# Kernel tuning notes

Measured on AMD Instinct MI355X. Metric: run time of the kernel, lower is better.

The kernel has to match this reference:

```python
import jax, jax.numpy as jnp
import numpy as np

BATCH = 256
INPUT_DIM = 64
LEVELS = 100
HV_DIM = 10000


def setup_inputs() -> dict:
    key = jax.random.key(0)
    kx, kb = jax.random.split(key)
    x = jax.random.uniform(kx, (BATCH, INPUT_DIM), dtype=jnp.float32)
    base = jax.random.normal(kb, (INPUT_DIM, LEVELS, HV_DIM), dtype=jnp.float32)
    # buffer is L2-normalized along hv_dim at construction time
    base = base / jnp.linalg.norm(base, axis=-1, keepdims=True)
    return {"x": x, "base_hvs": base}


def reference(x, base_hvs):
    D, L, H = base_hvs.shape
    B = x.shape[0]
    xn = jnp.clip(x * (L - 1), 0.0, float(L - 1))          # [B, D]
    lo = jnp.floor(xn).astype(jnp.int32)                    # [B, D]
    hi = jnp.clip(lo + 1, 0, L - 1)                         # [B, D]
    alpha = xn - lo.astype(x.dtype)                         # [B, D]

    def step(acc, inputs):
        bhv, l, h, a = inputs    # bhv: [L, H], l/h/a: [B]
        hv_low = bhv[l]          # [B, H] gather
        hv_high = bhv[h]         # [B, H] gather
        a = a[:, None]
        return acc + (1.0 - a) * hv_low + a * hv_high, None

    init = jnp.zeros((B, H), dtype=x.dtype)
    encoded, _ = jax.lax.scan(step, init, (base_hvs, lo.T, hi.T, alpha.T))
    return encoded / jnp.linalg.norm(encoded, axis=-1, keepdims=True)
```

## Files before the change

kernel.cpp:

```cpp
#include <hip/hip_runtime.h>
#include <hip/hip_bf16.h>

#define BATCH   256
#define DIMS    64
#define LEVELS  100
#define HVD     10000
#define WH      128
#define NHT     79
#define DSPLIT  8
#define DPER    8
#define TPB     512

typedef unsigned int  uint;
typedef unsigned short ushort;

#define PRM_OFF_BYTES (DSPLIT * BATCH * HVD * 2)

static __device__ __forceinline__ ushort f2bf(float f) {
    __hip_bfloat16 h = __float2bfloat16(f);
    return *reinterpret_cast<ushort*>(&h);
}

__global__ __launch_bounds__(256) void setup_kernel(
    const float* __restrict__ x, uint2* __restrict__ prm)
{
    const int i = blockIdx.x * 256 + threadIdx.x;
    if (i >= DIMS * BATCH) return;
    const int d = i >> 8;
    const int b = i & 255;
    float xv = x[b * DIMS + d];
    float xn = fminf(fmaxf(xv * (float)(LEVELS - 1), 0.0f), (float)(LEVELS - 1));
    float fl = floorf(xn);
    int   lo = (int)fl;
    int   hi = lo < LEVELS - 1 ? lo + 1 : LEVELS - 1;
    prm[i] = make_uint2((uint)(lo * WH * 4) | ((uint)(hi * WH * 4) << 16),
                        __float_as_uint(xn - fl));
}

__global__ __launch_bounds__(TPB, 4) void encode_kernel(
    const float* __restrict__ base,
    const uint2* __restrict__ prm,
    ushort*      __restrict__ partial)
{
    __shared__ float s_chunk[LEVELS * WH];

    const int tid   = threadIdx.x;
    const int w     = tid >> 6;
    const int lane  = tid & 63;
    const int htile = blockIdx.x;
    const int split = blockIdx.y;
    const int h0    = htile * WH;
    const int d0    = split * DPER;
    const int wvalid = (HVD - h0) < WH ? (HVD - h0) : WH;

    const int wu    = __builtin_amdgcn_readfirstlane(w);
    const int bbase = wu * 32;

    const int s   = lane >> 5;
    const int c   = lane & 31;
    const int cb  = c * 16;
    const int c4  = c * 4;
    const int srow = lane >> 5;
    const int scol = (lane & 31) * 4;

    float4 acc[16];
    #pragma unroll
    for (int j = 0; j < 16; ++j) acc[j] = make_float4(0.f, 0.f, 0.f, 0.f);

    #pragma unroll 1
    for (int dc = 0; dc < DPER; ++dc) {
        __syncthreads();

        const float* src = base + ((size_t)(d0 + dc) * LEVELS) * (size_t)HVD + h0;
        for (int p = w; p < LEVELS / 2; p += 8) {
            const float* g = src + (size_t)(2 * p + srow) * HVD + scol;
            if (scol < wvalid) {
                __builtin_amdgcn_global_load_lds(
                    (const __attribute__((address_space(1))) uint*)g,
                    (__attribute__((address_space(3))) uint*)&s_chunk[p * 2 * WH],
                    16, 0, 0);
            }
        }
        __syncthreads();

        const uint2* pr = prm + (size_t)(d0 + dc) * BATCH + bbase;

        #pragma unroll
        for (int jj = 0; jj < 16; ++jj) {
            const uint4 pq = *(const uint4*)(pr + 2 * jj);
            const uint  lohi = s ? pq.z : pq.x;
            const float a    = __uint_as_float(s ? pq.w : pq.y);
            const int   olo  = (int)(lohi & 0xffffu);
            const int   ohi  = (int)(lohi >> 16);
            const float4 vlo = *(const float4*)((const char*)s_chunk + olo + cb);
            const float4 vhi = *(const float4*)((const char*)s_chunk + ohi + cb);
            const float wl = 1.0f - a;
            acc[jj].x += wl * vlo.x + a * vhi.x;
            acc[jj].y += wl * vlo.y + a * vhi.y;
            acc[jj].z += wl * vlo.z + a * vhi.z;
            acc[jj].w += wl * vlo.w + a * vhi.w;
        }
    }

    if (c4 < wvalid) {
        #pragma unroll
        for (int jj = 0; jj < 16; ++jj) {
            const int b = bbase + 2 * jj + s;
            uint2 pk;
            pk.x = (uint)f2bf(acc[jj].x) | ((uint)f2bf(acc[jj].y) << 16);
            pk.y = (uint)f2bf(acc[jj].z) | ((uint)f2bf(acc[jj].w) << 16);
            *(uint2*)(partial + ((size_t)split * BATCH + b) * (size_t)HVD + h0 + c4) = pk;
        }
    }
}

__global__ __launch_bounds__(256) void finish_kernel(
    const ushort* __restrict__ partial,
    float* __restrict__ out)
{
    const int b   = blockIdx.x;
    const int tid = threadIdx.x;

    float ss = 0.f;
    for (int i = tid; i < HVD / 4; i += 256) {
        float4 sum = make_float4(0.f, 0.f, 0.f, 0.f);
        #pragma unroll
        for (int sp = 0; sp < DSPLIT; ++sp) {
            const uint2 u = *(const uint2*)(partial +
                ((size_t)sp * BATCH + b) * (size_t)HVD + i * 4);
            sum.x += __uint_as_float(u.x << 16);
            sum.y += __uint_as_float(u.x & 0xffff0000u);
            sum.z += __uint_as_float(u.y << 16);
            sum.w += __uint_as_float(u.y & 0xffff0000u);
        }
        *(float4*)(out + (size_t)b * HVD + i * 4) = sum;
        ss += sum.x * sum.x + sum.y * sum.y + sum.z * sum.z + sum.w * sum.w;
    }

    __shared__ float red[256];
    red[tid] = ss;
    __syncthreads();
    #pragma unroll
    for (int sh = 128; sh > 0; sh >>= 1) {
        if (tid < sh) red[tid] += red[tid + sh];
        __syncthreads();
    }
    const float inv = rsqrtf(red[0]);

    for (int i = tid; i < HVD / 4; i += 256) {
        float4 v = *(float4*)(out + (size_t)b * HVD + i * 4);
        v.x *= inv; v.y *= inv; v.z *= inv; v.w *= inv;
        *(float4*)(out + (size_t)b * HVD + i * 4) = v;
    }
}

extern "C" void kernel_launch(void* const* d_in, const int* in_sizes, int n_in,
                              void* d_out, int out_size, void* d_ws, size_t ws_size,
                              hipStream_t stream)
{
    const float* x    = (const float*)d_in[0];
    const float* base = (const float*)d_in[1];
    float*       out  = (float*)d_out;
    ushort*      part = (ushort*)d_ws;
    uint2*       prm  = (uint2*)((char*)d_ws + PRM_OFF_BYTES);

    setup_kernel<<<DIMS, 256, 0, stream>>>(x, prm);
    dim3 grid(NHT, DSPLIT);
    encode_kernel<<<grid, TPB, 0, stream>>>(base, prm, part);
    finish_kernel<<<BATCH, 256, 0, stream>>>(part, out);
}
```

Measured before the change: 383.4 us.

## Double-buffer LDS level chunks with async loads and narrower hv tiles

The encode kernel now uses 64-wide hv tiles and 256 threads per block. It keeps two LDS buffers so the global-to-LDS load for dimension dc+2 is in flight while dc is being accumulated, using vmcnt waits and raw barriers in place of full syncthreads. Per-sample parameters are packed into one 32-bit word (fp16 alpha plus 8-bit lo and hi indices) and staged once into LDS per block. This aims to hide global load latency behind compute, at the cost of reduced alpha precision, doubled LDS use per block, and narrower float2 LDS reads.

```diff
diff --git a/kernel.cpp b/kernel.cpp
--- a/kernel.cpp
+++ b/kernel.cpp
@@ -1,17 +1,20 @@
 #include <hip/hip_runtime.h>
+#include <hip/hip_fp16.h>
 #include <hip/hip_bf16.h>
 
 #define BATCH   256
 #define DIMS    64
 #define LEVELS  100
 #define HVD     10000
-#define WH      128
-#define NHT     79
+#define WH      64
+#define NHT     157
 #define DSPLIT  8
 #define DPER    8
-#define TPB     512
+#define TPB     256
+#define CHUNK_FLOATS (LEVELS * WH)
+#define NSTG    25
 
-typedef unsigned int  uint;
+typedef unsigned int   uint;
 typedef unsigned short ushort;
 
 #define PRM_OFF_BYTES (DSPLIT * BATCH * HVD * 2)
@@ -22,7 +25,7 @@
 }
 
 __global__ __launch_bounds__(256) void setup_kernel(
-    const float* __restrict__ x, uint2* __restrict__ prm)
+    const float* __restrict__ x, uint* __restrict__ prm)
 {
     const int i = blockIdx.x * 256 + threadIdx.x;
     if (i >= DIMS * BATCH) return;
@@ -33,16 +36,17 @@
     float fl = floorf(xn);
     int   lo = (int)fl;
     int   hi = lo < LEVELS - 1 ? lo + 1 : LEVELS - 1;
-    prm[i] = make_uint2((uint)(lo * WH * 4) | ((uint)(hi * WH * 4) << 16),
-                        __float_as_uint(xn - fl));
+    uint abits = (uint)__half_as_ushort(__float2half(xn - fl));
+    prm[i] = abits | ((uint)lo << 16) | ((uint)hi << 24);
 }
 
-__global__ __launch_bounds__(TPB, 4) void encode_kernel(
+__global__ __launch_bounds__(TPB, 2) void encode_kernel(
     const float* __restrict__ base,
-    const uint2* __restrict__ prm,
-    ushort*      __restrict__ partial)
+    const uint* __restrict__ prm,
+    ushort*     __restrict__ partial)
 {
-    __shared__ float s_chunk[LEVELS * WH];
+    __shared__ float s_buf[2][CHUNK_FLOATS];
+    __shared__ uint  s_prm[DPER][BATCH];
 
     const int tid   = threadIdx.x;
     const int w     = tid >> 6;
@@ -53,63 +57,74 @@
     const int d0    = split * DPER;
     const int wvalid = (HVD - h0) < WH ? (HVD - h0) : WH;
 
-    const int wu    = __builtin_amdgcn_readfirstlane(w);
-    const int bbase = wu * 32;
+    {
+        const uint4* pg = (const uint4*)(prm + d0 * BATCH);
+        uint4* pl = (uint4*)&s_prm[0][0];
+        for (int i = tid; i < DPER * BATCH / 4; i += TPB) pl[i] = pg[i];
+    }
+    __syncthreads();
 
-    const int s   = lane >> 5;
-    const int c   = lane & 31;
-    const int cb  = c * 16;
-    const int c4  = c * 4;
-    const int srow = lane >> 5;
-    const int scol = (lane & 31) * 4;
+    const int srow = lane >> 4;
+    const int scol = (lane & 15) * 4;
+    const float* srcdim = base + (size_t)d0 * LEVELS * HVD + h0;
 
-    float4 acc[16];
+    auto issue_chunk = [&](int dc, int bufidx) {
+        const float* src = srcdim + (size_t)dc * LEVELS * HVD;
+        float* dst = &s_buf[bufidx][0];
+        for (int p = w; p < NSTG; p += 4) {
+            const float* g = src + (size_t)(4 * p + srow) * HVD + scol;
+            if (scol < wvalid) {
+                __builtin_amdgcn_global_load_lds(
+                    (const __attribute__((address_space(1))) uint*)g,
+                    (__attribute__((address_space(3))) uint*)(dst + p * 4 * WH),
+                    16, 0, 0);
+            }
+        }
+    };
+
+    issue_chunk(0, 0);
+    issue_chunk(1, 1);
+
+    const int sub   = lane >> 5;
+    const int p2    = lane & 31;
+    const int pb    = p2 * 8;
+    const int bbase = w * 64;
+
+    float2 acc[32];
     #pragma unroll
-    for (int j = 0; j < 16; ++j) acc[j] = make_float4(0.f, 0.f, 0.f, 0.f);
+    for (int j = 0; j < 32; ++j) acc[j] = make_float2(0.f, 0.f);
 
     #pragma unroll 1
     for (int dc = 0; dc < DPER; ++dc) {
-        __syncthreads();
+        if (dc < DPER - 1) asm volatile("s_waitcnt vmcnt(6)" ::: "memory");
+        else               asm volatile("s_waitcnt vmcnt(0)" ::: "memory");
+        __builtin_amdgcn_s_barrier();
 
-        const float* src = base + ((size_t)(d0 + dc) * LEVELS) * (size_t)HVD + h0;
-        for (int p = w; p < LEVELS / 2; p += 8) {
-            const float* g = src + (size_t)(2 * p + srow) * HVD + scol;
-            if (scol < wvalid) {
-                __builtin_amdgcn_global_load_lds(
-                    (const __attribute__((address_space(1))) uint*)g,
-                    (__attribute__((address_space(3))) uint*)&s_chunk[p * 2 * WH],
-                    16, 0, 0);
-            }
+        const char* buf = (const char*)&s_buf[dc & 1][0];
+        #pragma unroll
+        for (int j = 0; j < 32; ++j) {
+            uint2 pp = *(const uint2*)&s_prm[dc][bbase + 2 * j];
+            const uint pk = sub ? pp.y : pp.x;
+            const float a = __half2float(__ushort_as_half((ushort)(pk & 0xffffu)));
+            const int olo = (int)((pk >> 16) & 0xffu) << 8;
+            const int ohi = (int)(pk >> 24) << 8;
+            const float2 vlo = *(const float2*)(buf + olo + pb);
+            const float2 vhi = *(const float2*)(buf + ohi + pb);
+            const float wl = 1.0f - a;
+            acc[j].x += wl * vlo.x + a * vhi.x;
+            acc[j].y += wl * vlo.y + a * vhi.y;
         }
-        __syncthreads();
-
-        const uint2* pr = prm + (size_t)(d0 + dc) * BATCH + bbase;
-
-        #pragma unroll
-        for (int jj = 0; jj < 16; ++jj) {
-            const uint4 pq = *(const uint4*)(pr + 2 * jj);
-            const uint  lohi = s ? pq.z : pq.x;
-            const float a    = __uint_as_float(s ? pq.w : pq.y);
-            const int   olo  = (int)(lohi & 0xffffu);
-            const int   ohi  = (int)(lohi >> 16);
-            const float4 vlo = *(const float4*)((const char*)s_chunk + olo + cb);
-            const float4 vhi = *(const float4*)((const char*)s_chunk + ohi + cb);
-            const float wl = 1.0f - a;
-            acc[jj].x += wl * vlo.x + a * vhi.x;
-            acc[jj].y += wl * vlo.y + a * vhi.y;
-            acc[jj].z += wl * vlo.z + a * vhi.z;
-            acc[jj].w += wl * vlo.w + a * vhi.w;
-        }
+        asm volatile("" ::: "memory");
+        __builtin_amdgcn_s_barrier();
+        if (dc < DPER - 2) issue_chunk(dc + 2, dc & 1);
     }
 
-    if (c4 < wvalid) {
+    if (p2 * 2 < wvalid) {
         #pragma unroll
-        for (int jj = 0; jj < 16; ++jj) {
-            const int b = bbase + 2 * jj + s;
-            uint2 pk;
-            pk.x = (uint)f2bf(acc[jj].x) | ((uint)f2bf(acc[jj].y) << 16);
-            pk.y = (uint)f2bf(acc[jj].z) | ((uint)f2bf(acc[jj].w) << 16);
-            *(uint2*)(partial + ((size_t)split * BATCH + b) * (size_t)HVD + h0 + c4) = pk;
+        for (int j = 0; j < 32; ++j) {
+            const int b = bbase + 2 * j + sub;
+            const uint pk = (uint)f2bf(acc[j].x) | ((uint)f2bf(acc[j].y) << 16);
+            *(uint*)(partial + ((size_t)split * BATCH + b) * (size_t)HVD + h0 + p2 * 2) = pk;
         }
     }
 }
@@ -162,7 +177,7 @@
     const float* base = (const float*)d_in[1];
     float*       out  = (float*)d_out;
     ushort*      part = (ushort*)d_ws;
-    uint2*       prm  = (uint2*)((char*)d_ws + PRM_OFF_BYTES);
+    uint*        prm  = (uint*)((char*)d_ws + PRM_OFF_BYTES);
 
     setup_kernel<<<DIMS, 256, 0, stream>>>(x, prm);
     dim3 grid(NHT, DSPLIT);
```

After: 381.4 us. About the same (-0.5%).
